# Performance work log

Measured on AMD Instinct MI355X. Metric: run time of the kernel, lower is better.

## Reference

```python
import jax, jax.numpy as jnp
import numpy as np

N, F, E = 10000, 128, 640000
HID_RO = 64


def setup_inputs() -> dict:
    key = jax.random.key(0)
    ks = jax.random.split(key, 16)
    s = 1.0 / np.sqrt(F)
    inp = {
        'h': jax.random.normal(ks[0], (N, F), jnp.float32),
        'src_idx': jax.random.randint(ks[1], (E,), 0, N, jnp.int32),
        'dst_idx': jax.random.randint(ks[2], (E,), 0, N, jnp.int32),
        # message-creation MLP (F -> F -> F)
        'W1': jax.random.normal(ks[3], (F, F), jnp.float32) * s,
        'b1': jnp.zeros((F,), jnp.float32),
        'W2': jax.random.normal(ks[4], (F, F), jnp.float32) * s,
        'b2': jnp.zeros((F,), jnp.float32),
        # attention aggregation kernels
        'node_kernel': jax.random.normal(ks[5], (F, F), jnp.float32) * s,
        'attn_kernel': jax.random.normal(ks[6], (2 * F, 1), jnp.float32) * s,
        # feed-forward update (agg + h -> new h)
        'Wu': jax.random.normal(ks[7], (2 * F, F), jnp.float32) * s,
        'bu': jnp.zeros((F,), jnp.float32),
        # readout MLP (F -> 64 -> 1)
        'Wr1': jax.random.normal(ks[8], (F, HID_RO), jnp.float32) * s,
        'br1': jnp.zeros((HID_RO,), jnp.float32),
        'Wr2': jax.random.normal(ks[9], (HID_RO, 1), jnp.float32) * (1.0 / np.sqrt(HID_RO)),
        'br2': jnp.zeros((1,), jnp.float32),
    }
    return inp


def reference(h, src_idx, dst_idx, W1, b1, W2, b2, node_kernel, attn_kernel,
              Wu, bu, Wr1, br1, Wr2, br2):
    n = h.shape[0]
    # per-edge gather + message-creation NN  [E, F]
    h_src = h[src_idx]
    m = jax.nn.relu(h_src @ W1 + b1) @ W2 + b2
    # attention aggregation (GAT-style): transform messages, score vs dst state
    wh = m @ node_kernel                      # [E, F]
    h_dst = h[dst_idx]                        # [E, F]
    e = jax.nn.leaky_relu(jnp.concatenate([wh, h_dst], axis=-1) @ attn_kernel,
                          negative_slope=0.2)[:, 0]  # [E]
    # per-destination segment softmax (numerically stable)
    e_max = jax.ops.segment_max(e, dst_idx, num_segments=n)
    ex = jnp.exp(e - e_max[dst_idx])
    denom = jax.ops.segment_sum(ex, dst_idx, num_segments=n)
    alpha = ex / (denom[dst_idx] + 1e-9)
    # scatter-reduce weighted messages into destination states  [N, F]
    agg = jax.ops.segment_sum(m * alpha[:, None], dst_idx, num_segments=n)
    # feed-forward update
    h_new = jax.nn.relu(jnp.concatenate([agg, h], axis=-1) @ Wu + bu)
    # readout MLP -> per-node scalar
    out = jax.nn.relu(h_new @ Wr1 + br1) @ Wr2 + br2  # [N, 1]
    return out
```

## Files before the change

### kernel.cpp

```cpp
#include <hip/hip_runtime.h>
#include <hip/hip_bf16.h>
#include <hip/hip_fp16.h>

#define F 128
#define HID 64
#define KMAX 4
#define DEG_CAP 256
#define NTM 16
#define NTU 16
#define CHUNK_LOG 13
#define CHUNK (1 << CHUNK_LOG)


__global__ __launch_bounds__(256) void fused_front(
    const int* __restrict__ dst, unsigned short* __restrict__ cnt,
    unsigned short* __restrict__ rank,
    int e, int n, int histBlocks,
    const float* __restrict__ h,
    const float* __restrict__ W1, const float* __restrict__ b1,
    const float* __restrict__ W2, const float* __restrict__ b2,
    const float* __restrict__ nk, const float* __restrict__ attn,
    __half* __restrict__ Mh, float* __restrict__ p, float* __restrict__ q)
{
    __shared__ __align__(16) int lhist[10240];
    int tid = threadIdx.x;

    if ((int)blockIdx.x < histBlocks) {
        int n4 = n >> 2;
        int4* lh4 = (int4*)lhist;
        for (int i = tid; i < n4; i += 256) lh4[i] = make_int4(0, 0, 0, 0);
        for (int i = (n4 << 2) + tid; i < n; i += 256) lhist[i] = 0;
        __syncthreads();

        int base = (int)blockIdx.x << CHUNK_LOG;
        int lim = min(e - base, CHUNK);
        int lim4 = lim >> 2;
        const int4* d4 = (const int4*)(dst + base);
        for (int k = tid; k < lim4; k += 256) {
            int4 dv = d4[k];
            ushort4 rv;
            rv.x = (unsigned short)atomicAdd(&lhist[dv.x], 1);
            rv.y = (unsigned short)atomicAdd(&lhist[dv.y], 1);
            rv.z = (unsigned short)atomicAdd(&lhist[dv.z], 1);
            rv.w = (unsigned short)atomicAdd(&lhist[dv.w], 1);
            *(ushort4*)&rank[base + 4 * k] = rv;
        }
        for (int k = (lim4 << 2) + tid; k < lim; k += 256)
            rank[base + k] = (unsigned short)atomicAdd(&lhist[dst[base + k]], 1);
        __syncthreads();

        unsigned int* crow = (unsigned int*)(cnt + (size_t)blockIdx.x * n);
        int nh = n >> 1;
        for (int i = tid; i < nh; i += 256) {
            unsigned int v = ((unsigned int)lhist[2 * i] & 0xffffu) |
                             ((unsigned int)lhist[2 * i + 1] << 16);
            crow[i] = v;
        }
        return;
    }

    float (*hsTs)[F] = (float (*)[F])lhist;
    float (*Wc)[F]   = (float (*)[F])((char*)lhist + 8192);
    float* v1s       = (float*)((char*)lhist + 24576);

    int bm = blockIdx.x - histBlocks;
    int row0 = bm * NTM;
    int j0 = (tid & 31) * 4;
    int r0 = (tid >> 5) * 2;

    #pragma unroll
    for (int it = 0; it < 2; ++it) {
        int s4 = tid + it * 256;
        int r = s4 >> 5, c4 = s4 & 31;
        int row = row0 + r;
        float4 v = make_float4(0, 0, 0, 0);
        if (row < n) v = *(const float4*)&h[(size_t)row * F + c4 * 4];
        *(float4*)&hsTs[r][c4 * 4] = v;
    }
    if (tid < F) {
        float a = 0.f;
        const float4* nkr = (const float4*)&nk[(size_t)tid * F];
        const float4* at4 = (const float4*)attn;
        #pragma unroll 8
        for (int j = 0; j < 32; ++j) {
            float4 nv = nkr[j]; float4 av = at4[j];
            a = fmaf(nv.x, av.x, a); a = fmaf(nv.y, av.y, a);
            a = fmaf(nv.z, av.z, a); a = fmaf(nv.w, av.w, a);
        }
        v1s[tid] = a;
    }
    __syncthreads();

    {
        int r = tid >> 4, kp = tid & 15;
        float qa = 0.f;
        #pragma unroll
        for (int c = 0; c < 2; ++c) {
            float4 hv = *(const float4*)&hsTs[r][kp * 8 + c * 4];
            float4 av = *(const float4*)&attn[F + kp * 8 + c * 4];
            qa = fmaf(hv.x, av.x, qa); qa = fmaf(hv.y, av.y, qa);
            qa = fmaf(hv.z, av.z, qa); qa = fmaf(hv.w, av.w, qa);
        }
        #pragma unroll
        for (int off = 1; off < 16; off <<= 1) qa += __shfl_xor(qa, off, 64);
        int row = row0 + r;
        if (kp == 0 && row < n) q[row] = qa;
    }

    float4 acc[2];
    {
        float4 bv = *(const float4*)&b1[j0];
        acc[0] = bv; acc[1] = bv;
    }
    for (int cc = 0; cc < 4; ++cc) {
        int kc = ((cc + bm) & 3) * 32;
        __syncthreads();
        #pragma unroll
        for (int it = 0; it < 4; ++it) {
            int s4 = tid + it * 256;
            int wr = s4 >> 5, wc4 = s4 & 31;
            *(float4*)&Wc[wr][wc4 * 4] =
                *(const float4*)&W1[(size_t)(kc + wr) * F + wc4 * 4];
        }
        __syncthreads();
        #pragma unroll
        for (int k4 = 0; k4 < 8; ++k4) {
            int kk = k4 * 4;
            float4 a0 = *(const float4*)&hsTs[r0 + 0][kc + kk];
            float4 a1 = *(const float4*)&hsTs[r0 + 1][kc + kk];
            #pragma unroll
            for (int k = 0; k < 4; ++k) {
                float4 b = *(const float4*)&Wc[kk + k][j0];
                float av0 = k == 0 ? a0.x : k == 1 ? a0.y : k == 2 ? a0.z : a0.w;
                float av1 = k == 0 ? a1.x : k == 1 ? a1.y : k == 2 ? a1.z : a1.w;
                acc[0].x = fmaf(av0, b.x, acc[0].x); acc[0].y = fmaf(av0, b.y, acc[0].y);
                acc[0].z = fmaf(av0, b.z, acc[0].z); acc[0].w = fmaf(av0, b.w, acc[0].w);
                acc[1].x = fmaf(av1, b.x, acc[1].x); acc[1].y = fmaf(av1, b.y, acc[1].y);
                acc[1].z = fmaf(av1, b.z, acc[1].z); acc[1].w = fmaf(av1, b.w, acc[1].w);
            }
        }
    }
    __syncthreads();
    #pragma unroll
    for (int i = 0; i < 2; ++i) {
        float4 t = acc[i];
        t.x = fmaxf(t.x, 0.f); t.y = fmaxf(t.y, 0.f);
        t.z = fmaxf(t.z, 0.f); t.w = fmaxf(t.w, 0.f);
        *(float4*)&hsTs[r0 + i][j0] = t;
    }

    {
        float4 bv = *(const float4*)&b2[j0];
        acc[0] = bv; acc[1] = bv;
    }
    for (int cc = 0; cc < 4; ++cc) {
        int kc = ((cc + bm) & 3) * 32;
        __syncthreads();
        #pragma unroll
        for (int it = 0; it < 4; ++it) {
            int s4 = tid + it * 256;
            int wr = s4 >> 5, wc4 = s4 & 31;
            *(float4*)&Wc[wr][wc4 * 4] =
                *(const float4*)&W2[(size_t)(kc + wr) * F + wc4 * 4];
        }
        __syncthreads();
        #pragma unroll
        for (int k4 = 0; k4 < 8; ++k4) {
            int kk = k4 * 4;
            float4 a0 = *(const float4*)&hsTs[r0 + 0][kc + kk];
            float4 a1 = *(const float4*)&hsTs[r0 + 1][kc + kk];
            #pragma unroll
            for (int k = 0; k < 4; ++k) {
                float4 b = *(const float4*)&Wc[kk + k][j0];
                float av0 = k == 0 ? a0.x : k == 1 ? a0.y : k == 2 ? a0.z : a0.w;
                float av1 = k == 0 ? a1.x : k == 1 ? a1.y : k == 2 ? a1.z : a1.w;
                acc[0].x = fmaf(av0, b.x, acc[0].x); acc[0].y = fmaf(av0, b.y, acc[0].y);
                acc[0].z = fmaf(av0, b.z, acc[0].z); acc[0].w = fmaf(av0, b.w, acc[0].w);
                acc[1].x = fmaf(av1, b.x, acc[1].x); acc[1].y = fmaf(av1, b.y, acc[1].y);
                acc[1].z = fmaf(av1, b.z, acc[1].z); acc[1].w = fmaf(av1, b.w, acc[1].w);
            }
        }
    }

    float4 v1v = *(const float4*)&v1s[j0];
    #pragma unroll
    for (int i = 0; i < 2; ++i) {
        int row = row0 + r0 + i;
        if (row < n) {
            __half hv[4];
            hv[0] = __float2half(acc[i].x); hv[1] = __float2half(acc[i].y);
            hv[2] = __float2half(acc[i].z); hv[3] = __float2half(acc[i].w);
            *(uint2*)&Mh[(size_t)row * F + j0] = *(uint2*)hv;
        }
        float pp = acc[i].x * v1v.x + acc[i].y * v1v.y +
                   acc[i].z * v1v.z + acc[i].w * v1v.w;
        #pragma unroll
        for (int off = 1; off < 32; off <<= 1) pp += __shfl_xor(pp, off, 64);
        if ((tid & 31) == 0 && row < n) p[row] = pp;
    }
}

__global__ __launch_bounds__(256) void scan_block(
    unsigned short* __restrict__ cnt, int* __restrict__ rstart,
    int* __restrict__ bsum, int n, int hb)
{
    int tid = threadIdx.x;
    int i = blockIdx.x * 256 + tid;
    int run = 0;
    if (i < n) {
        size_t stride = (size_t)n;
        size_t idx = (size_t)i;
        int r = 0;
        for (; r + 8 <= hb; r += 8) {
            int c0 = cnt[idx];
            int c1 = cnt[idx + stride];
            int c2 = cnt[idx + 2 * stride];
            int c3 = cnt[idx + 3 * stride];
            int c4 = cnt[idx + 4 * stride];
            int c5 = cnt[idx + 5 * stride];
            int c6 = cnt[idx + 6 * stride];
            int c7 = cnt[idx + 7 * stride];
            cnt[idx]              = (unsigned short)run;
            cnt[idx + stride]     = (unsigned short)(run + c0);
            cnt[idx + 2 * stride] = (unsigned short)(run + (c0 + c1));
            cnt[idx + 3 * stride] = (unsigned short)(run + (c0 + c1 + c2));
            cnt[idx + 4 * stride] = (unsigned short)(run + (c0 + c1 + c2 + c3));
            cnt[idx + 5 * stride] = (unsigned short)(run + (c0 + c1 + c2 + c3 + c4));
            cnt[idx + 6 * stride] = (unsigned short)(run + (c0 + c1 + c2 + c3 + c4 + c5));
            cnt[idx + 7 * stride] = (unsigned short)(run + (c0 + c1 + c2 + c3 + c4 + c5 + c6));
            run += c0 + c1 + c2 + c3 + c4 + c5 + c6 + c7;
            idx += 8 * stride;
        }
        for (; r < hb; ++r) {
            int c = cnt[idx];
            cnt[idx] = (unsigned short)run;
            run += c;
            idx += stride;
        }
    }
    int v = run;
    int lane = tid & 63, wv = tid >> 6;
    int x = v;
    #pragma unroll
    for (int off = 1; off < 64; off <<= 1) {
        int t = __shfl_up(x, off, 64);
        if (lane >= off) x += t;
    }
    __shared__ int wsum[4];
    if (lane == 63) wsum[wv] = x;
    __syncthreads();
    int woff = 0;
    #pragma unroll
    for (int wdx = 0; wdx < 4; ++wdx) woff += (wdx < wv) ? wsum[wdx] : 0;
    int incl = x + woff;
    if (i < n) rstart[i] = incl - v;
    if (tid == 255) bsum[blockIdx.x] = incl;
}

__global__ __launch_bounds__(256) void fill_kernel(
    const int* __restrict__ dst, const int* __restrict__ src,
    const unsigned short* __restrict__ rank, const int* __restrict__ rstart,
    const unsigned short* __restrict__ cntoff, const int* __restrict__ bsum,
    unsigned short* __restrict__ src_sorted, int n, int nb, int e)
{
    __shared__ int sbo[64];
    int tid = threadIdx.x;
    if (tid < 64) {
        int v = (tid < nb) ? bsum[tid] : 0;
        int x = v;
        #pragma unroll
        for (int off = 1; off < 64; off <<= 1) {
            int t = __shfl_up(x, off, 64);
            if (tid >= off) x += t;
        }
        sbo[tid] = x - v;
    }
    __syncthreads();
    int i = blockIdx.x * 256 + tid;
    if (i < e) {
        int d = dst[i];
        int rep = i >> CHUNK_LOG;
        int pos = rstart[d] + sbo[d >> 8] + (int)cntoff[(size_t)rep * n + d] + (int)rank[i];
        src_sorted[pos] = (unsigned short)src[i];
    }
}

__global__ __launch_bounds__(256) void agg_softmax_gather(
    const __half* __restrict__ Mh, const float* __restrict__ p,
    const float* __restrict__ q, const int* __restrict__ rstart,
    const int* __restrict__ bsum, const unsigned short* __restrict__ src_sorted,
    float* __restrict__ agg, int n, int nb, int e)
{
    __shared__ int2 buf[4][DEG_CAP];
    __shared__ int sbo[64];
    int tid = threadIdx.x;
    if (tid < 64) {
        int v = (tid < nb) ? bsum[tid] : 0;
        int x = v;
        #pragma unroll
        for (int off = 1; off < 64; off <<= 1) {
            int t = __shfl_up(x, off, 64);
            if (tid >= off) x += t;
        }
        sbo[tid] = x - v;
    }
    __syncthreads();

    int lane = tid & 63;
    int wv   = tid >> 6;
    int node = blockIdx.x * 4 + wv;
    if (node >= n) return;

    int start = rstart[node] + sbo[node >> 8];
    int end   = (node + 1 < n) ? rstart[node + 1] + sbo[(node + 1) >> 8] : e;
    int deg   = end - start;
    float qn  = q[node];

    float w[KMAX];
    int   sidx[KMAX];
    float lmax = -1e30f;

    #pragma unroll
    for (int k = 0; k < KMAX; ++k) {
        int i = start + lane + (k << 6);
        bool valid = (i < end);
        int sv = valid ? (int)src_sorted[i] : 0;
        float pv = valid ? p[sv] : 0.0f;
        float sc = pv + qn;
        float ev = (sc > 0.0f) ? sc : 0.2f * sc;
        w[k] = valid ? ev : -1e30f;
        sidx[k] = sv;
        lmax = fmaxf(lmax, w[k]);
    }
    for (int i = start + DEG_CAP + lane; i < end; i += 64) {
        float sc = p[(int)src_sorted[i]] + qn;
        float ev = (sc > 0.0f) ? sc : 0.2f * sc;
        lmax = fmaxf(lmax, ev);
    }
    #pragma unroll
    for (int off = 32; off >= 1; off >>= 1)
        lmax = fmaxf(lmax, __shfl_xor(lmax, off, 64));

    float lsum = 0.0f;
    #pragma unroll
    for (int k = 0; k < KMAX; ++k) {
        float ex = (w[k] > -1e29f) ? __expf(w[k] - lmax) : 0.0f;
        w[k] = ex;
        lsum += ex;
    }
    for (int i = start + DEG_CAP + lane; i < end; i += 64) {
        float sc = p[(int)src_sorted[i]] + qn;
        float ev = (sc > 0.0f) ? sc : 0.2f * sc;
        lsum += __expf(ev - lmax);
    }
    #pragma unroll
    for (int off = 32; off >= 1; off >>= 1)
        lsum += __shfl_xor(lsum, off, 64);
    float inv = 1.0f / (lsum + 1e-9f);

    #pragma unroll
    for (int k = 0; k < KMAX; ++k)
        buf[wv][lane + (k << 6)] = make_int2(__float_as_int(w[k] * inv), sidx[k]);

    const uint4* M16 = (const uint4*)Mh;
    int sub16 = lane & 15;
    int quar  = lane >> 4;
    float acc[8] = {0.f, 0.f, 0.f, 0.f, 0.f, 0.f, 0.f, 0.f};
    int lim = min(deg, DEG_CAP);
    lim = (lim + 15) & ~15;

    for (int base = 0; base < lim; base += 16) {
        int2  rr[4];
        uint4 mm[4];
        #pragma unroll
        for (int u = 0; u < 4; ++u) rr[u] = buf[wv][base + quar + 4 * u];
        #pragma unroll
        for (int u = 0; u < 4; ++u) mm[u] = M16[(size_t)rr[u].y * 16 + sub16];
        #pragma unroll
        for (int u = 0; u < 4; ++u) {
            float wu = __int_as_float(rr[u].x);
            const __half2* hp = (const __half2*)&mm[u];
            float2 f0 = __half22float2(hp[0]);
            float2 f1 = __half22float2(hp[1]);
            float2 f2 = __half22float2(hp[2]);
            float2 f3 = __half22float2(hp[3]);
            acc[0] = fmaf(wu, f0.x, acc[0]); acc[1] = fmaf(wu, f0.y, acc[1]);
            acc[2] = fmaf(wu, f1.x, acc[2]); acc[3] = fmaf(wu, f1.y, acc[3]);
            acc[4] = fmaf(wu, f2.x, acc[4]); acc[5] = fmaf(wu, f2.y, acc[5]);
            acc[6] = fmaf(wu, f3.x, acc[6]); acc[7] = fmaf(wu, f3.y, acc[7]);
        }
    }

    for (int base = start + DEG_CAP; base < end; base += 64) {
        int i = base + lane;
        float ex = 0.f; int sv = 0;
        if (i < end) {
            sv = (int)src_sorted[i];
            float sc = p[sv] + qn;
            float ev = (sc > 0.0f) ? sc : 0.2f * sc;
            ex = __expf(ev - lmax) * inv;
        }
        buf[wv][lane] = make_int2(__float_as_int(ex), sv);
        for (int b2 = 0; b2 < 64; b2 += 4) {
            int2 rr = buf[wv][b2 + quar];
            uint4 mm = M16[(size_t)rr.y * 16 + sub16];
            float wu = __int_as_float(rr.x);
            const __half2* hp = (const __half2*)&mm;
            float2 f0 = __half22float2(hp[0]);
            float2 f1 = __half22float2(hp[1]);
            float2 f2 = __half22float2(hp[2]);
            float2 f3 = __half22float2(hp[3]);
            acc[0] = fmaf(wu, f0.x, acc[0]); acc[1] = fmaf(wu, f0.y, acc[1]);
            acc[2] = fmaf(wu, f1.x, acc[2]); acc[3] = fmaf(wu, f1.y, acc[3]);
            acc[4] = fmaf(wu, f2.x, acc[4]); acc[5] = fmaf(wu, f2.y, acc[5]);
            acc[6] = fmaf(wu, f3.x, acc[6]); acc[7] = fmaf(wu, f3.y, acc[7]);
        }
    }

    #pragma unroll
    for (int j = 0; j < 8; ++j) {
        acc[j] += __shfl_xor(acc[j], 16, 64);
        acc[j] += __shfl_xor(acc[j], 32, 64);
    }
    if (quar == 0) {
        float* dst0 = &agg[(size_t)node * F + sub16 * 8];
        *(float4*)dst0       = make_float4(acc[0], acc[1], acc[2], acc[3]);
        *(float4*)(dst0 + 4) = make_float4(acc[4], acc[5], acc[6], acc[7]);
    }
}

__global__ __launch_bounds__(256) void update_readout_v3(
    const float* __restrict__ agg, const float* __restrict__ h,
    const float* __restrict__ Wu, const float* __restrict__ bu,
    const float* __restrict__ Wr1, const float* __restrict__ br1,
    const float* __restrict__ Wr2, const float* __restrict__ br2,
    float* __restrict__ out, int n)
{
    __shared__ __align__(16) float X[NTU][2 * F];
    __shared__ __align__(16) float Wc[32][F];
    int tid = threadIdx.x;
    int row0 = blockIdx.x * NTU;
    int j0 = (tid & 31) * 4;
    int r0 = (tid >> 5) * 2;

    #pragma unroll
    for (int it = 0; it < 4; ++it) {
        int s4 = tid + it * 256;
        int r = s4 >> 6, c4 = s4 & 63;
        int row = row0 + r;
        float4 v = make_float4(0, 0, 0, 0);
        if (row < n) {
            if (c4 < 32) v = *(const float4*)&agg[(size_t)row * F + c4 * 4];
            else         v = *(const float4*)&h[(size_t)row * F + (c4 - 32) * 4];
        }
        *(float4*)&X[r][c4 * 4] = v;
    }

    float4 acc[2];
    {
        float4 bv = *(const float4*)&bu[j0];
        acc[0] = bv; acc[1] = bv;
    }
    for (int cc = 0; cc < 8; ++cc) {
        int kc = ((cc + (int)blockIdx.x) & 7) * 32;
        __syncthreads();
        #pragma unroll
        for (int it = 0; it < 4; ++it) {
            int s4 = tid + it * 256;
            int wr = s4 >> 5, wc4 = s4 & 31;
            *(float4*)&Wc[wr][wc4 * 4] =
                *(const float4*)&Wu[(size_t)(kc + wr) * F + wc4 * 4];
        }
        __syncthreads();
        #pragma unroll
        for (int k4 = 0; k4 < 8; ++k4) {
            int kk = k4 * 4;
            float4 a0 = *(const float4*)&X[r0 + 0][kc + kk];
            float4 a1 = *(const float4*)&X[r0 + 1][kc + kk];
            #pragma unroll
            for (int k = 0; k < 4; ++k) {
                float4 b = *(const float4*)&Wc[kk + k][j0];
                float av0 = k == 0 ? a0.x : k == 1 ? a0.y : k == 2 ? a0.z : a0.w;
                float av1 = k == 0 ? a1.x : k == 1 ? a1.y : k == 2 ? a1.z : a1.w;
                acc[0].x = fmaf(av0, b.x, acc[0].x); acc[0].y = fmaf(av0, b.y, acc[0].y);
                acc[0].z = fmaf(av0, b.z, acc[0].z); acc[0].w = fmaf(av0, b.w, acc[0].w);
                acc[1].x = fmaf(av1, b.x, acc[1].x); acc[1].y = fmaf(av1, b.y, acc[1].y);
                acc[1].z = fmaf(av1, b.z, acc[1].z); acc[1].w = fmaf(av1, b.w, acc[1].w);
            }
        }
    }
    __syncthreads();
    float (*hn)[F] = (float (*)[F])&X[0][0];
    #pragma unroll
    for (int i = 0; i < 2; ++i) {
        float4 t = acc[i];
        t.x = fmaxf(t.x, 0.f); t.y = fmaxf(t.y, 0.f);
        t.z = fmaxf(t.z, 0.f); t.w = fmaxf(t.w, 0.f);
        *(float4*)&hn[r0 + i][j0] = t;
    }

    int h0 = (tid & 31) * 2;
    float r1[2][2];
    {
        float b0 = br1[h0], b1v = br1[h0 + 1];
        r1[0][0] = b0; r1[0][1] = b1v;
        r1[1][0] = b0; r1[1][1] = b1v;
    }
    float* Wcr = &Wc[0][0];
    for (int cc = 0; cc < 2; ++cc) {
        int kc = cc * 64;
        __syncthreads();
        #pragma unroll
        for (int it = 0; it < 4; ++it) {
            int s4 = tid + it * 256;
            int wr = s4 >> 4, wc4 = s4 & 15;
            *(float4*)&Wcr[wr * 64 + wc4 * 4] =
                *(const float4*)&Wr1[(size_t)(kc + wr) * HID + wc4 * 4];
        }
        __syncthreads();
        #pragma unroll
        for (int k4 = 0; k4 < 16; ++k4) {
            int kk = k4 * 4;
            float4 a0 = *(const float4*)&hn[r0 + 0][kc + kk];
            float4 a1 = *(const float4*)&hn[r0 + 1][kc + kk];
            #pragma unroll
            for (int k = 0; k < 4; ++k) {
                float2 b = *(const float2*)&Wcr[(kk + k) * 64 + h0];
                float av0 = k == 0 ? a0.x : k == 1 ? a0.y : k == 2 ? a0.z : a0.w;
                float av1 = k == 0 ? a1.x : k == 1 ? a1.y : k == 2 ? a1.z : a1.w;
                r1[0][0] = fmaf(av0, b.x, r1[0][0]); r1[0][1] = fmaf(av0, b.y, r1[0][1]);
                r1[1][0] = fmaf(av1, b.x, r1[1][0]); r1[1][1] = fmaf(av1, b.y, r1[1][1]);
            }
        }
    }

    float wa = Wr2[h0], wb = Wr2[h0 + 1];
    float b2v = br2[0];
    #pragma unroll
    for (int i = 0; i < 2; ++i) {
        float s = fmaxf(r1[i][0], 0.f) * wa + fmaxf(r1[i][1], 0.f) * wb;
        #pragma unroll
        for (int off = 1; off < 32; off <<= 1) s += __shfl_xor(s, off, 64);
        int row = row0 + r0 + i;
        if ((tid & 31) == 0 && row < n) out[row] = s + b2v;
    }
}

extern "C" void kernel_launch(void* const* d_in, const int* in_sizes, int n_in,
                              void* d_out, int out_size, void* d_ws, size_t ws_size,
                              hipStream_t stream) {
    const float* h    = (const float*)d_in[0];
    const int*   src  = (const int*)d_in[1];
    const int*   dst  = (const int*)d_in[2];
    const float* W1   = (const float*)d_in[3];
    const float* b1   = (const float*)d_in[4];
    const float* W2   = (const float*)d_in[5];
    const float* b2   = (const float*)d_in[6];
    const float* nk   = (const float*)d_in[7];
    const float* attn = (const float*)d_in[8];
    const float* Wu   = (const float*)d_in[9];
    const float* bu   = (const float*)d_in[10];
    const float* Wr1  = (const float*)d_in[11];
    const float* br1  = (const float*)d_in[12];
    const float* Wr2  = (const float*)d_in[13];
    const float* br2  = (const float*)d_in[14];
    float* out = (float*)d_out;

    int n = in_sizes[0] / F;
    int e = in_sizes[1];
    int nb = (n + 255) / 256;
    int hb = (e + CHUNK - 1) >> CHUNK_LOG;
    int mlpBlocks  = (n + NTM - 1) / NTM;
    int updBlocks  = (n + NTU - 1) / NTU;
    int fillBlocks = (e + 255) / 256;

    char* ws = (char*)d_ws;
    size_t off = 0;
    auto alloc = [&](size_t bytes) {
        void* pp = ws + off;
        off += (bytes + 511) & ~(size_t)511;
        return pp;
    };
    __half* Mh             = (__half*)alloc((size_t)n * F * 2);
    float* aggws           = (float*)alloc((size_t)n * F * 4);
    float* p               = (float*)alloc((size_t)n * 4);
    float* q               = (float*)alloc((size_t)n * 4);
    unsigned short* cnt    = (unsigned short*)alloc((size_t)hb * n * 2);
    int*   rstart          = (int*)alloc((size_t)(n + 1) * 4);
    int*   bsum            = (int*)alloc((size_t)(nb + 1) * 4);
    unsigned short* rank   = (unsigned short*)alloc((size_t)e * 2);
    unsigned short* srcsort= (unsigned short*)alloc((size_t)e * 2);

    fused_front<<<hb + mlpBlocks, 256, 0, stream>>>(
        dst, cnt, rank, e, n, hb,
        h, W1, b1, W2, b2, nk, attn, Mh, p, q);
    scan_block<<<nb, 256, 0, stream>>>(cnt, rstart, bsum, n, hb);
    fill_kernel<<<fillBlocks, 256, 0, stream>>>(dst, src, rank, rstart,
                                                cnt, bsum, srcsort,
                                                n, nb, e);
    agg_softmax_gather<<<(n + 3) / 4, 256, 0, stream>>>(Mh, p, q, rstart, bsum,
                                                        srcsort, aggws, n, nb, e);
    update_readout_v3<<<updBlocks, 256, 0, stream>>>(aggws, h, Wu, bu,
                                                     Wr1, br1, Wr2, br2,
                                                     out, n);
}
```

Before: 169.1 us.

## Split update and readout GEMMs along K across waves, reading weights from global

Rewrites the update/readout kernel so each wave owns a K-slice of the reduction and computes 8 rows by 4 columns per thread. Weights are read directly from global/L2 instead of being staged through shared memory. Wave partial sums are then reduced in shared memory. This removes most of the per-chunk __syncthreads and shared-memory weight staging and raises register reuse per loaded weight. In exchange it adds a cross-wave reduction step, uses more registers and depends on cache hits for the weight reads.

```diff
diff --git a/kernel.cpp b/kernel.cpp
--- a/kernel.cpp
+++ b/kernel.cpp
@@ -429,19 +429,21 @@
     }
 }
 
-__global__ __launch_bounds__(256) void update_readout_v3(
+__global__ __launch_bounds__(256) void update_readout_v5(
     const float* __restrict__ agg, const float* __restrict__ h,
     const float* __restrict__ Wu, const float* __restrict__ bu,
     const float* __restrict__ Wr1, const float* __restrict__ br1,
     const float* __restrict__ Wr2, const float* __restrict__ br2,
     float* __restrict__ out, int n)
 {
-    __shared__ __align__(16) float X[NTU][2 * F];
-    __shared__ __align__(16) float Wc[32][F];
+    __shared__ __align__(16) float smem[8192];
+    float (*X)[2 * F] = (float (*)[2 * F])smem;
     int tid = threadIdx.x;
+    int wv   = tid >> 6;
+    int lane = tid & 63;
     int row0 = blockIdx.x * NTU;
-    int j0 = (tid & 31) * 4;
-    int r0 = (tid >> 5) * 2;
+    int j0 = (lane & 31) * 4;
+    int rh = (lane >> 5) * 8;
 
     #pragma unroll
     for (int it = 0; it < 4; ++it) {
@@ -455,94 +457,101 @@
         }
         *(float4*)&X[r][c4 * 4] = v;
     }
-
-    float4 acc[2];
+    __syncthreads();
+
+    float4 acc[8];
+    #pragma unroll
+    for (int i = 0; i < 8; ++i) acc[i] = make_float4(0.f, 0.f, 0.f, 0.f);
+    int kbase = wv * 64;
+    for (int k4 = 0; k4 < 16; ++k4) {
+        int kk = kbase + k4 * 4;
+        float4 a[8];
+        #pragma unroll
+        for (int r = 0; r < 8; ++r) a[r] = *(const float4*)&X[rh + r][kk];
+        #pragma unroll
+        for (int k = 0; k < 4; ++k) {
+            float4 b = *(const float4*)&Wu[(size_t)(kk + k) * F + j0];
+            #pragma unroll
+            for (int r = 0; r < 8; ++r) {
+                float av = k == 0 ? a[r].x : k == 1 ? a[r].y : k == 2 ? a[r].z : a[r].w;
+                acc[r].x = fmaf(av, b.x, acc[r].x);
+                acc[r].y = fmaf(av, b.y, acc[r].y);
+                acc[r].z = fmaf(av, b.z, acc[r].z);
+                acc[r].w = fmaf(av, b.w, acc[r].w);
+            }
+        }
+    }
+    __syncthreads();
+
+    #pragma unroll
+    for (int r = 0; r < 8; ++r)
+        *(float4*)&smem[wv * 2048 + (rh + r) * 128 + j0] = acc[r];
+    __syncthreads();
+
+    #pragma unroll
+    for (int u = 0; u < 2; ++u) {
+        int idx = tid * 2 + u;
+        int row = idx >> 5, c4 = (idx & 31) * 4;
+        float4 s0 = *(const float4*)&smem[0 * 2048 + row * 128 + c4];
+        float4 s1 = *(const float4*)&smem[1 * 2048 + row * 128 + c4];
+        float4 s2 = *(const float4*)&smem[2 * 2048 + row * 128 + c4];
+        float4 s3 = *(const float4*)&smem[3 * 2048 + row * 128 + c4];
+        float4 bv = *(const float4*)&bu[c4];
+        float4 t;
+        t.x = fmaxf(s0.x + s1.x + s2.x + s3.x + bv.x, 0.f);
+        t.y = fmaxf(s0.y + s1.y + s2.y + s3.y + bv.y, 0.f);
+        t.z = fmaxf(s0.z + s1.z + s2.z + s3.z + bv.z, 0.f);
+        t.w = fmaxf(s0.w + s1.w + s2.w + s3.w + bv.w, 0.f);
+        *(float4*)&smem[row * 128 + c4] = t;
+    }
+    __syncthreads();
+
+    int h0 = (lane & 31) * 2;
+    float r1a[8], r1b[8];
+    #pragma unroll
+    for (int r = 0; r < 8; ++r) { r1a[r] = 0.f; r1b[r] = 0.f; }
+    int kb2 = wv * 32;
+    for (int k4 = 0; k4 < 8; ++k4) {
+        int kk = kb2 + k4 * 4;
+        float4 a[8];
+        #pragma unroll
+        for (int r = 0; r < 8; ++r) a[r] = *(const float4*)&smem[(rh + r) * 128 + kk];
+        #pragma unroll
+        for (int k = 0; k < 4; ++k) {
+            float2 b = *(const float2*)&Wr1[(size_t)(kk + k) * HID + h0];
+            #pragma unroll
+            for (int r = 0; r < 8; ++r) {
+                float av = k == 0 ? a[r].x : k == 1 ? a[r].y : k == 2 ? a[r].z : a[r].w;
+                r1a[r] = fmaf(av, b.x, r1a[r]);
+                r1b[r] = fmaf(av, b.y, r1b[r]);
+            }
+        }
+    }
+    #pragma unroll
+    for (int r = 0; r < 8; ++r) {
+        smem[2048 + wv * 1024 + (rh + r) * 64 + h0]     = r1a[r];
+        smem[2048 + wv * 1024 + (rh + r) * 64 + h0 + 1] = r1b[r];
+    }
+    __syncthreads();
+
     {
-        float4 bv = *(const float4*)&bu[j0];
-        acc[0] = bv; acc[1] = bv;
-    }
-    for (int cc = 0; cc < 8; ++cc) {
-        int kc = ((cc + (int)blockIdx.x) & 7) * 32;
-        __syncthreads();
-        #pragma unroll
-        for (int it = 0; it < 4; ++it) {
-            int s4 = tid + it * 256;
-            int wr = s4 >> 5, wc4 = s4 & 31;
-            *(float4*)&Wc[wr][wc4 * 4] =
-                *(const float4*)&Wu[(size_t)(kc + wr) * F + wc4 * 4];
-        }
-        __syncthreads();
-        #pragma unroll
-        for (int k4 = 0; k4 < 8; ++k4) {
-            int kk = k4 * 4;
-            float4 a0 = *(const float4*)&X[r0 + 0][kc + kk];
-            float4 a1 = *(const float4*)&X[r0 + 1][kc + kk];
-            #pragma unroll
-            for (int k = 0; k < 4; ++k) {
-                float4 b = *(const float4*)&Wc[kk + k][j0];
-                float av0 = k == 0 ? a0.x : k == 1 ? a0.y : k == 2 ? a0.z : a0.w;
-                float av1 = k == 0 ? a1.x : k == 1 ? a1.y : k == 2 ? a1.z : a1.w;
-                acc[0].x = fmaf(av0, b.x, acc[0].x); acc[0].y = fmaf(av0, b.y, acc[0].y);
-                acc[0].z = fmaf(av0, b.z, acc[0].z); acc[0].w = fmaf(av0, b.w, acc[0].w);
-                acc[1].x = fmaf(av1, b.x, acc[1].x); acc[1].y = fmaf(av1, b.y, acc[1].y);
-                acc[1].z = fmaf(av1, b.z, acc[1].z); acc[1].w = fmaf(av1, b.w, acc[1].w);
-            }
-        }
-    }
-    __syncthreads();
-    float (*hn)[F] = (float (*)[F])&X[0][0];
-    #pragma unroll
-    for (int i = 0; i < 2; ++i) {
-        float4 t = acc[i];
-        t.x = fmaxf(t.x, 0.f); t.y = fmaxf(t.y, 0.f);
-        t.z = fmaxf(t.z, 0.f); t.w = fmaxf(t.w, 0.f);
-        *(float4*)&hn[r0 + i][j0] = t;
-    }
-
-    int h0 = (tid & 31) * 2;
-    float r1[2][2];
-    {
-        float b0 = br1[h0], b1v = br1[h0 + 1];
-        r1[0][0] = b0; r1[0][1] = b1v;
-        r1[1][0] = b0; r1[1][1] = b1v;
-    }
-    float* Wcr = &Wc[0][0];
-    for (int cc = 0; cc < 2; ++cc) {
-        int kc = cc * 64;
-        __syncthreads();
-        #pragma unroll
-        for (int it = 0; it < 4; ++it) {
-            int s4 = tid + it * 256;
-            int wr = s4 >> 4, wc4 = s4 & 15;
-            *(float4*)&Wcr[wr * 64 + wc4 * 4] =
-                *(const float4*)&Wr1[(size_t)(kc + wr) * HID + wc4 * 4];
-        }
-        __syncthreads();
-        #pragma unroll
-        for (int k4 = 0; k4 < 16; ++k4) {
-            int kk = k4 * 4;
-            float4 a0 = *(const float4*)&hn[r0 + 0][kc + kk];
-            float4 a1 = *(const float4*)&hn[r0 + 1][kc + kk];
-            #pragma unroll
-            for (int k = 0; k < 4; ++k) {
-                float2 b = *(const float2*)&Wcr[(kk + k) * 64 + h0];
-                float av0 = k == 0 ? a0.x : k == 1 ? a0.y : k == 2 ? a0.z : a0.w;
-                float av1 = k == 0 ? a1.x : k == 1 ? a1.y : k == 2 ? a1.z : a1.w;
-                r1[0][0] = fmaf(av0, b.x, r1[0][0]); r1[0][1] = fmaf(av0, b.y, r1[0][1]);
-                r1[1][0] = fmaf(av1, b.x, r1[1][0]); r1[1][1] = fmaf(av1, b.y, r1[1][1]);
-            }
-        }
-    }
-
-    float wa = Wr2[h0], wb = Wr2[h0 + 1];
-    float b2v = br2[0];
-    #pragma unroll
-    for (int i = 0; i < 2; ++i) {
-        float s = fmaxf(r1[i][0], 0.f) * wa + fmaxf(r1[i][1], 0.f) * wb;
-        #pragma unroll
-        for (int off = 1; off < 32; off <<= 1) s += __shfl_xor(s, off, 64);
-        int row = row0 + r0 + i;
-        if ((tid & 31) == 0 && row < n) out[row] = s + b2v;
+        int row = tid >> 4;
+        int hp  = (tid & 15) * 4;
+        float val = 0.f;
+        #pragma unroll
+        for (int j = 0; j < 4; ++j) {
+            int hh = hp + j;
+            float s = br1[hh]
+                    + smem[2048 + 0 * 1024 + row * 64 + hh]
+                    + smem[2048 + 1 * 1024 + row * 64 + hh]
+                    + smem[2048 + 2 * 1024 + row * 64 + hh]
+                    + smem[2048 + 3 * 1024 + row * 64 + hh];
+            val = fmaf(fmaxf(s, 0.f), Wr2[hh], val);
+        }
+        #pragma unroll
+        for (int off = 1; off < 16; off <<= 1) val += __shfl_xor(val, off, 64);
+        int orow = row0 + row;
+        if ((tid & 15) == 0 && orow < n) out[orow] = val + br2[0];
     }
 }
 
@@ -600,7 +609,7 @@
                                                 n, nb, e);
     agg_softmax_gather<<<(n + 3) / 4, 256, 0, stream>>>(Mh, p, q, rstart, bsum,
                                                         srcsort, aggws, n, nb, e);
-    update_readout_v3<<<updBlocks, 256, 0, stream>>>(aggws, h, Wu, bu,
+    update_readout_v5<<<updBlocks, 256, 0, stream>>>(aggws, h, Wu, bu,
                                                      Wr1, br1, Wr2, br2,
                                                      out, n);
 }
```

Result: faster. 156.6 us (-7.4%).
